# Optimization experiments

Hardware: AMD Instinct MI355X
Metric: run time of the kernel (lower is better)

The kernel has to match this reference:

```python
import jax, jax.numpy as jnp
import numpy as np
import math

N, C, W = 4, 768, 2048
H = 12            # num_attention_heads
D = C // H        # attention_head_size = 64
G = 4             # q/k/v groups


def grouped_conv1x1(x, w, b):
    # x: [N, C, W]; w: [G, C/G, C/G] (cout_per_g, cin_per_g); b: [C]
    xg = x.reshape(N, G, C // G, W)
    out = jnp.einsum('goc,ngcw->ngow', w, xg)       # [N, G, C/G, W]
    return out.reshape(N, C, W) + b[None, :, None]


def setup_inputs() -> dict:
    key = jax.random.key(0)
    ks = jax.random.split(key, 7)
    s = 1.0 / math.sqrt(C // G)
    return {
        'hidden_states': jax.random.normal(ks[0], (N, C, W), jnp.float32),
        'attention_mask': jnp.zeros((N, 1, 1, W), jnp.float32),
        'wq': jax.random.normal(ks[1], (G, C // G, C // G), jnp.float32) * s,
        'bq': jax.random.normal(ks[2], (C,), jnp.float32) * 0.02,
        'wk': jax.random.normal(ks[3], (G, C // G, C // G), jnp.float32) * s,
        'bk': jax.random.normal(ks[4], (C,), jnp.float32) * 0.02,
        'wv': jax.random.normal(ks[5], (G, C // G, C // G), jnp.float32) * s,
        'bv': jax.random.normal(ks[6], (C,), jnp.float32) * 0.02,
    }


def reference(hidden_states, attention_mask, wq, bq, wk, bk, wv, bv):
    q = grouped_conv1x1(hidden_states, wq, bq)       # [N, C, W]
    k = grouped_conv1x1(hidden_states, wk, bk)
    v = grouped_conv1x1(hidden_states, wv, bv)
    # transpose_for_scores_conv1d: [N,C,W] -> [N,H,W,D]
    q = q.reshape(N, H, D, W).transpose(0, 1, 3, 2)
    # transpose_key_for_scores_conv1d: [N,C,W] -> [N,H,D,W]
    k = k.reshape(N, H, D, W)
    v = v.reshape(N, H, D, W).transpose(0, 1, 3, 2)
    scores = jnp.einsum('nhqd,nhdk->nhqk', q, k) / math.sqrt(D)
    scores = scores + attention_mask                 # broadcast [N,1,1,W]
    probs = jax.nn.softmax(scores, axis=-1)          # dropout p=0 (eval)
    ctx = jnp.einsum('nhqk,nhkd->nhqd', probs, v)    # [N,H,W,D]
    # transpose_output_conv1d: [N,H,W,D] -> [N,C,W]
    return ctx.transpose(0, 1, 3, 2).reshape(N, C, W)
```

## Files before the change

### kernel.cpp

```cpp
#include <hip/hip_runtime.h>
#include <math.h>

typedef __attribute__((ext_vector_type(4))) float floatx4;
typedef __attribute__((ext_vector_type(8))) short shortx8;
typedef __attribute__((ext_vector_type(4))) short shortx4;

#define NB 4
#define CC 768
#define WW 2048
#define HH 12
#define DD 64
#define GG 4
#define CG 192
#define HPG 3
#define L2E 1.4426950408889634f
#define C18 0.18033688011112043f
#define MSH 11.541560327111707f
#define WSZ (GG * CG * CG)

__device__ __forceinline__ float fast_exp2(float x) {
    return __builtin_amdgcn_exp2f(x);
}

__device__ __forceinline__ short f2bf(float f) {
    union { float f; unsigned u; } v; v.f = f;
    unsigned r = v.u + 0x7fffu + ((v.u >> 16) & 1u);
    return (short)(r >> 16);
}

template<int CTRL>
__device__ __forceinline__ float dppror(float v) {
    return __int_as_float(__builtin_amdgcn_update_dpp(
        0, __float_as_int(v), CTRL, 0xf, 0xf, false));
}
__device__ __forceinline__ float rsum16(float v) {
    v += dppror<0x128>(v);
    v += dppror<0x124>(v);
    v += dppror<0x122>(v);
    v += dppror<0x121>(v);
    return v;
}

__device__ __forceinline__ void gl_lds16(const void* g, void* l) {
    __builtin_amdgcn_global_load_lds(
        (const __attribute__((address_space(1))) unsigned int*)g,
        (__attribute__((address_space(3))) unsigned int*)l, 16, 0, 0);
}

__global__ __launch_bounds__(256) void prep(
    const float* __restrict__ x,
    const float* __restrict__ wq, const float* __restrict__ wk,
    const float* __restrict__ wv,
    short* __restrict__ XTh, short* __restrict__ Wf)
{
    __shared__ short Th[64 * 72];
    const int tid = threadIdx.x;
    const int b   = blockIdx.x;

    if (b < 1536) {
        const int w0 = (b & 31) * 64;
        const int c0 = ((b >> 5) % 12) * 64;
        const int n  = b / 384;
        const int w  = tid & 63;
        const int cb = (tid >> 6) * 16;

        float xv[16];
        #pragma unroll
        for (int j = 0; j < 16; ++j)
            xv[j] = x[((size_t)n * CC + c0 + cb + j) * WW + w0 + w];

        shortx8 hi0, hi1;
        #pragma unroll
        for (int j = 0; j < 8; ++j) { hi0[j] = f2bf(xv[j]); hi1[j] = f2bf(xv[j + 8]); }
        *(shortx8*)&Th[w * 72 + cb]     = hi0;
        *(shortx8*)&Th[w * 72 + cb + 8] = hi1;
        __syncthreads();

        const int wr = tid >> 2;
        const int cc = (tid & 3) * 16;
        const size_t ro = ((size_t)n * WW + w0 + wr) * CC + c0 + cc;
        *(shortx8*)&XTh[ro]     = *(const shortx8*)&Th[wr * 72 + cc];
        *(shortx8*)&XTh[ro + 8] = *(const shortx8*)&Th[wr * 72 + cc + 8];
    } else {
        const int t = (b - 1536) * 256 + tid;
        const int g  = t / (CG * CG);
        const int r  = t - g * (CG * CG);
        const int o  = r / CG;
        const int k  = r - o * CG;
        const int off = (((g * 12 + (o >> 4)) * 6 + (k >> 5)) * 512)
                      + ((k >> 3) & 3) * 128 + (o & 15) * 8 + (k & 7);
        const float* src[3] = {wq, wk, wv};
        #pragma unroll
        for (int m = 0; m < 3; ++m)
            Wf[m * WSZ + off] = f2bf(src[m][t]);
    }
}

__global__ __launch_bounds__(256) void qkv_gemm(
    const short* __restrict__ XTh, const short* __restrict__ Wf,
    const float* __restrict__ bq, const float* __restrict__ bk,
    const float* __restrict__ bv,
    short* __restrict__ Qb, short* __restrict__ Kb, short* __restrict__ Vb)
{
    __shared__ __align__(16) char smem[26112];
    short* Xh_l = (short*)smem;

    const int lin  = blockIdx.x;
    const int xcd  = lin & 7;
    const int iw   = lin >> 3;
    const int mat  = iw % 3;
    const int tile = (iw / 3) * 8 + xcd;
    const int p0   = (tile & 31) * 64;
    const int g    = (tile >> 5) & 3;
    const int n    = tile >> 7;

    const int tid  = threadIdx.x;
    const int wid  = __builtin_amdgcn_readfirstlane(tid >> 6);
    const int lane = tid & 63;
    const int l15  = lane & 15;
    const int quad = lane >> 4;
    const int ob   = wid * 48;

    {
        const short* xhb = XTh + ((size_t)n * WW + p0) * CC + g * CG;
        #pragma unroll
        for (int rd = 0; rd < 6; ++rd) {
            const int Lb = rd * 256 + wid * 64;
            const int L  = Lb + lane;
            const int p  = (L * 2731) >> 16;
            const int sc = L - p * 24;
            const int ss = (sc & ~7) | ((sc & 7) ^ (p & 7));
            gl_lds16(xhb + (size_t)p * CC + ss * 8, &Xh_l[Lb * 8]);
        }
    }
    __syncthreads();

    floatx4 acc[3][4];
    #pragma unroll
    for (int mi = 0; mi < 3; ++mi)
        #pragma unroll
        for (int ni = 0; ni < 4; ++ni) acc[mi][ni] = (floatx4)0.0f;

    const short* wfm = Wf + (size_t)mat * WSZ + lane * 8;

    #pragma unroll
    for (int ks = 0; ks < 6; ++ks) {
        shortx8 ah[3], bh[4];
        #pragma unroll
        for (int mi = 0; mi < 3; ++mi)
            ah[mi] = *(const shortx8*)(wfm + (((g * 12 + wid * 3 + mi) * 6 + ks) << 9));
        #pragma unroll
        for (int ni = 0; ni < 4; ++ni) {
            const int p  = ni * 16 + l15;
            const int vp = (ks >> 1) * 8 + ((((ks & 1) * 4) + quad) ^ (p & 7));
            bh[ni] = *(const shortx8*)&Xh_l[(p * 24 + vp) * 8];
        }
        #pragma unroll
        for (int mi = 0; mi < 3; ++mi)
            #pragma unroll
            for (int ni = 0; ni < 4; ++ni)
                acc[mi][ni] = __builtin_amdgcn_mfma_f32_16x16x32_bf16(ah[mi], bh[ni], acc[mi][ni], 0, 0, 0);
    }

    const float* bias = (mat == 0) ? bq : (mat == 1) ? bk : bv;
    short* Y = (mat == 0) ? Qb : (mat == 1) ? Kb : Vb;

    __syncthreads();

    if (mat < 2) {
        short* T = (short*)smem;
        #pragma unroll
        for (int mi = 0; mi < 3; ++mi) {
            float4 b4 = *(const float4*)&bias[g * CG + ob + mi * 16 + quad * 4];
            const int o = ob + mi * 16 + quad * 4;
            #pragma unroll
            for (int ni = 0; ni < 4; ++ni) {
                const int p = ni * 16 + l15;
                T[p * 200 + o]     = f2bf(acc[mi][ni][0] + b4.x);
                T[p * 200 + o + 1] = f2bf(acc[mi][ni][1] + b4.y);
                T[p * 200 + o + 2] = f2bf(acc[mi][ni][2] + b4.z);
                T[p * 200 + o + 3] = f2bf(acc[mi][ni][3] + b4.w);
            }
        }
        __syncthreads();
        #pragma unroll
        for (int hc = 0; hc < HPG; ++hc) {
            const size_t nh = (size_t)n * HH + g * HPG + hc;
            #pragma unroll
            for (int half = 0; half < 2; ++half) {
                const int idx = tid + half * 256;
                const int p  = idx >> 3;
                const int dc = (idx & 7) * 8;
                *(shortx8*)&Y[(nh * WW + p0 + p) * DD + dc] =
                    *(const shortx8*)&T[p * 200 + hc * 64 + dc];
            }
        }
    } else {
        short* T = (short*)smem;
        #pragma unroll
        for (int mi = 0; mi < 3; ++mi) {
            float4 b4 = *(const float4*)&bias[g * CG + ob + mi * 16 + quad * 4];
            const int o = ob + mi * 16 + quad * 4;
            #pragma unroll
            for (int ni = 0; ni < 4; ++ni) {
                const int p = ni * 16 + l15;
                T[(o)     * 68 + p] = f2bf(acc[mi][ni][0] + b4.x);
                T[(o + 1) * 68 + p] = f2bf(acc[mi][ni][1] + b4.y);
                T[(o + 2) * 68 + p] = f2bf(acc[mi][ni][2] + b4.z);
                T[(o + 3) * 68 + p] = f2bf(acc[mi][ni][3] + b4.w);
            }
        }
        __syncthreads();
        #pragma unroll
        for (int pass = 0; pass < 6; ++pass) {
            const int idx = tid + pass * 256;
            const int o  = idx >> 3;
            const int pc = (idx & 7) * 8;
            const size_t nh = (size_t)n * HH + g * HPG + (o >> 6);
            const int d = o & 63;
            *(shortx8*)&Y[(nh * DD + d) * WW + p0 + pc] =
                *(const shortx8*)&T[o * 68 + pc];
        }
    }
}

#define PST 72
#define RST 65

__global__ __launch_bounds__(256) void attn_split(
    const short* __restrict__ Qb, const short* __restrict__ Kb,
    const short* __restrict__ Vb, const float* __restrict__ mask,
    float* __restrict__ out)
{
    __shared__ __align__(16) char smem[50176];
    short* Pl = (short*)(smem + 32768);
    float* Ml = (float*)(smem + 41984);

    const int lin  = blockIdx.x;
    const int xcd  = lin & 7;
    const int slot = lin >> 3;
    const int pair = xcd * 6 + (slot >> 5);
    const int qt   = slot & 31;
    const int n    = pair / HH;
    const int h    = pair % HH;
    const int q0   = qt * 64;

    const int tid  = threadIdx.x;
    const int wid  = __builtin_amdgcn_readfirstlane(tid >> 6);
    const int lane = tid & 63;
    const int l15  = lane & 15;
    const int quad = lane >> 4;

    const size_t nh = (size_t)n * HH + h;
    const short* Kbase = Kb + nh * WW * DD;
    const short* Vbase = Vb + nh * DD * WW;

    {
        const float* mbase = mask + (size_t)n * WW;
        #pragma unroll
        for (int i = 0; i < WW / 256; ++i)
            Ml[tid + i * 256] = fmaf(mbase[tid + i * 256], L2E, -MSH);
    }

    shortx8 qf[2];
    {
        const short* qp = Qb + (nh * WW + q0 + wid * 16 + l15) * DD + quad * 8;
        qf[0] = *(const shortx8*)(qp);
        qf[1] = *(const shortx8*)(qp + 32);
    }

    floatx4 oacc[4];
    #pragma unroll
    for (int nn2 = 0; nn2 < 4; ++nn2) oacc[nn2] = (floatx4)0.0f;
    float lst[4] = {0.f, 0.f, 0.f, 0.f};

    short* Pw = Pl + wid * 16 * PST;

    const int r0  = wid * 16 + (lane >> 3);
    const int r1  = r0 + 8;
    const int cg0 = (lane & 7) ^ (r0 & 7);
    const int cg1 = (lane & 7) ^ (r1 & 7);
    const short* kp0 = Kbase + (size_t)r0 * DD + cg0 * 8;
    const short* kp1 = Kbase + (size_t)r1 * DD + cg1 * 8;
    const short* vp0 = Vbase + (size_t)r0 * WW + cg0 * 8;
    const short* vp1 = Vbase + (size_t)r1 * WW + cg1 * 8;
    const int KR0 = (wid * 16) * 64, KR1 = (wid * 16 + 8) * 64;

    #define STAGE(j, bb)                                                      \
        do {                                                                  \
            short* ksd = (short*)(smem + (bb) * 8192);                        \
            short* vsd = (short*)(smem + 16384 + (bb) * 8192);                \
            gl_lds16(kp0 + (size_t)(j) * 64 * DD, ksd + KR0);                 \
            gl_lds16(kp1 + (size_t)(j) * 64 * DD, ksd + KR1);                 \
            gl_lds16(vp0 + (j) * 64, vsd + KR0);                              \
            gl_lds16(vp1 + (j) * 64, vsd + KR1);                              \
        } while (0)

    STAGE(0, 0);
    __syncthreads();

    for (int kt = 0; kt < WW / 64; ++kt) {
        const int bb = kt & 1;
        if (kt + 1 < WW / 64) STAGE(kt + 1, 1 - bb);

        const short* Ks_l = (const short*)(smem + bb * 8192);
        const short* Vs_l = (const short*)(smem + 16384 + bb * 8192);
        const int k0 = kt * 64;

        shortx8 kf[4][2], vf[4][2];
        #pragma unroll
        for (int jj = 0; jj < 4; ++jj) {
            const int r = 16 * jj + l15;
            #pragma unroll
            for (int hf = 0; hf < 2; ++hf)
                kf[jj][hf] = *(const shortx8*)&Ks_l[r * 64 + (((hf * 4 + quad) ^ (r & 7)) * 8)];
        }
        #pragma unroll
        for (int nn2 = 0; nn2 < 4; ++nn2) {
            const int r = 16 * nn2 + l15;
            #pragma unroll
            for (int hf = 0; hf < 2; ++hf)
                vf[nn2][hf] = *(const shortx8*)&Vs_l[r * 64 + (((hf * 4 + quad) ^ (r & 7)) * 8)];
        }
        float mv2[4];
        #pragma unroll
        for (int jj = 0; jj < 4; ++jj)
            mv2[jj] = Ml[k0 + 16 * jj + l15];

        floatx4 sacc[4];
        #pragma unroll
        for (int jj = 0; jj < 4; ++jj) {
            sacc[jj] = (floatx4)0.0f;
            sacc[jj] = __builtin_amdgcn_mfma_f32_16x16x32_bf16(qf[0], kf[jj][0], sacc[jj], 0, 0, 0);
            sacc[jj] = __builtin_amdgcn_mfma_f32_16x16x32_bf16(qf[1], kf[jj][1], sacc[jj], 0, 0, 0);
        }

        #pragma unroll
        for (int jj = 0; jj < 4; ++jj) {
            #pragma unroll
            for (int r = 0; r < 4; ++r) {
                float p = fast_exp2(fmaf(sacc[jj][r], C18, mv2[jj]));
                lst[r] += p;
                Pw[(quad * 4 + r) * PST + 16 * jj + l15] = f2bf(p);
            }
        }

        shortx8 pf0 = *(const shortx8*)&Pw[l15 * PST + quad * 8];
        shortx8 pf1 = *(const shortx8*)&Pw[l15 * PST + 32 + quad * 8];

        #pragma unroll
        for (int nn2 = 0; nn2 < 4; ++nn2) {
            oacc[nn2] = __builtin_amdgcn_mfma_f32_16x16x32_bf16(pf0, vf[nn2][0], oacc[nn2], 0, 0, 0);
            oacc[nn2] = __builtin_amdgcn_mfma_f32_16x16x32_bf16(pf1, vf[nn2][1], oacc[nn2], 0, 0, 0);
        }
        __syncthreads();
    }
    #undef STAGE

    float linv[4];
    #pragma unroll
    for (int r = 0; r < 4; ++r) linv[r] = 1.0f / rsum16(lst[r]);

    float* Ol = (float*)smem;
    #pragma unroll
    for (int nn2 = 0; nn2 < 4; ++nn2)
        #pragma unroll
        for (int r = 0; r < 4; ++r)
            Ol[(wid * 16 + quad * 4 + r) * RST + nn2 * 16 + l15] = oacc[nn2][r] * linv[r];
    __syncthreads();

    float* obase = out + (nh * DD) * WW + q0;
    #pragma unroll
    for (int it = 0; it < 4; ++it) {
        const int idx = tid + it * 256;
        const int q4 = (idx & 15) * 4;
        const int d  = idx >> 4;
        floatx4 v;
        #pragma unroll
        for (int i = 0; i < 4; ++i) v[i] = Ol[(q4 + i) * RST + d];
        *(floatx4*)&obase[(size_t)d * WW + q4] = v;
    }
}

extern "C" void kernel_launch(void* const* d_in, const int* in_sizes, int n_in,
                              void* d_out, int out_size, void* d_ws, size_t ws_size,
                              hipStream_t stream) {
    const float* x    = (const float*)d_in[0];
    const float* mask = (const float*)d_in[1];
    const float* wq   = (const float*)d_in[2];
    const float* bq   = (const float*)d_in[3];
    const float* wk   = (const float*)d_in[4];
    const float* bk   = (const float*)d_in[5];
    const float* wv   = (const float*)d_in[6];
    const float* bv   = (const float*)d_in[7];
    float* out = (float*)d_out;

    const size_t per = (size_t)NB * HH * WW * DD;
    short* Qb  = (short*)d_ws;
    short* Kb  = Qb + per;
    short* Vb  = Kb + per;
    short* XTh = Vb + per;
    short* Wfp = XTh + per;

    hipLaunchKernelGGL(prep, dim3(1536 + WSZ / 256), dim3(256), 0, stream,
                       x, wq, wk, wv, XTh, Wfp);
    hipLaunchKernelGGL(qkv_gemm, dim3(1536), dim3(256), 0, stream,
                       XTh, Wfp, bq, bk, bv, Qb, Kb, Vb);
    hipLaunchKernelGGL(attn_split, dim3(1536), dim3(256), 0, stream,
                       Qb, Kb, Vb, mask, out);
}
```

Before: 190.7 us.

## Keep softmax probabilities in registers via transposed QK MFMA and row-permuted K

Computes S^T by swapping MFMA operands and permuting the K rows loaded from LDS, so each lane's exp outputs already form the A-operand layout of the PV MFMA. The LDS round-trip for P is removed, the bf16 conversion uses packed v_cvt_pk_bf16_f32, and row sums are taken with an extra MFMA against a vector of ones instead of DPP reductions. A new LDS swizzle (swz8) and vectorized mask loads go with the new row mapping. This trades two extra MFMAs per tile and bf16-rounded row sums for fewer LDS writes and reads and less VALU work.

```diff
diff --git a/kernel.cpp b/kernel.cpp
--- a/kernel.cpp
+++ b/kernel.cpp
@@ -28,17 +28,20 @@
     return (short)(r >> 16);
 }
 
-template<int CTRL>
-__device__ __forceinline__ float dppror(float v) {
-    return __int_as_float(__builtin_amdgcn_update_dpp(
-        0, __float_as_int(v), CTRL, 0xf, 0xf, false));
-}
-__device__ __forceinline__ float rsum16(float v) {
-    v += dppror<0x128>(v);
-    v += dppror<0x124>(v);
-    v += dppror<0x122>(v);
-    v += dppror<0x121>(v);
-    return v;
+__device__ __forceinline__ int cvtpk(float lo, float hi) {
+    int r;
+    asm("v_cvt_pk_bf16_f32 %0, %1, %2" : "=v"(r) : "v"(lo), "v"(hi));
+    return r;
+}
+
+__device__ __forceinline__ shortx8 mk8(int a, int b, int c, int d) {
+    union { int i[4]; shortx8 h; } u;
+    u.i[0] = a; u.i[1] = b; u.i[2] = c; u.i[3] = d;
+    return u.h;
+}
+
+__device__ __forceinline__ int swz8(int r) {
+    return (((r & 7) * 2) + ((r >> 3) & 1)) & 7;
 }
 
 __device__ __forceinline__ void gl_lds16(const void* g, void* l) {
@@ -224,7 +227,6 @@
     }
 }
 
-#define PST 72
 #define RST 65
 
 __global__ __launch_bounds__(256) void attn_split(
@@ -232,9 +234,8 @@
     const short* __restrict__ Vb, const float* __restrict__ mask,
     float* __restrict__ out)
 {
-    __shared__ __align__(16) char smem[50176];
-    short* Pl = (short*)(smem + 32768);
-    float* Ml = (float*)(smem + 41984);
+    __shared__ __align__(16) char smem[40960];
+    float* Ml = (float*)(smem + 32768);
 
     const int lin  = blockIdx.x;
     const int xcd  = lin & 7;
@@ -269,22 +270,26 @@
         qf[1] = *(const shortx8*)(qp + 32);
     }
 
+    shortx8 onef;
+    #pragma unroll
+    for (int j = 0; j < 8; ++j) onef[j] = (short)0x3F80;
+
     floatx4 oacc[4];
     #pragma unroll
     for (int nn2 = 0; nn2 < 4; ++nn2) oacc[nn2] = (floatx4)0.0f;
-    float lst[4] = {0.f, 0.f, 0.f, 0.f};
-
-    short* Pw = Pl + wid * 16 * PST;
+    floatx4 lsum = (floatx4)0.0f;
 
     const int r0  = wid * 16 + (lane >> 3);
     const int r1  = r0 + 8;
-    const int cg0 = (lane & 7) ^ (r0 & 7);
-    const int cg1 = (lane & 7) ^ (r1 & 7);
+    const int cg0 = (lane & 7) ^ swz8(r0);
+    const int cg1 = (lane & 7) ^ swz8(r1);
     const short* kp0 = Kbase + (size_t)r0 * DD + cg0 * 8;
     const short* kp1 = Kbase + (size_t)r1 * DD + cg1 * 8;
     const short* vp0 = Vbase + (size_t)r0 * WW + cg0 * 8;
     const short* vp1 = Vbase + (size_t)r1 * WW + cg1 * 8;
     const int KR0 = (wid * 16) * 64, KR1 = (wid * 16 + 8) * 64;
+
+    const int rowmap = (l15 >> 2) * 8 + (l15 & 3);
 
     #define STAGE(j, bb)                                                      \
         do {                                                                  \
@@ -310,56 +315,62 @@
         shortx8 kf[4][2], vf[4][2];
         #pragma unroll
         for (int jj = 0; jj < 4; ++jj) {
-            const int r = 16 * jj + l15;
+            const int rp = ((jj >> 1) * 32) + ((jj & 1) * 4) + rowmap;
             #pragma unroll
             for (int hf = 0; hf < 2; ++hf)
-                kf[jj][hf] = *(const shortx8*)&Ks_l[r * 64 + (((hf * 4 + quad) ^ (r & 7)) * 8)];
+                kf[jj][hf] = *(const shortx8*)&Ks_l[rp * 64 + (((hf * 4 + quad) ^ swz8(rp)) * 8)];
         }
         #pragma unroll
         for (int nn2 = 0; nn2 < 4; ++nn2) {
             const int r = 16 * nn2 + l15;
             #pragma unroll
             for (int hf = 0; hf < 2; ++hf)
-                vf[nn2][hf] = *(const shortx8*)&Vs_l[r * 64 + (((hf * 4 + quad) ^ (r & 7)) * 8)];
-        }
-        float mv2[4];
-        #pragma unroll
-        for (int jj = 0; jj < 4; ++jj)
-            mv2[jj] = Ml[k0 + 16 * jj + l15];
+                vf[nn2][hf] = *(const shortx8*)&Vs_l[r * 64 + (((hf * 4 + quad) ^ swz8(r)) * 8)];
+        }
+
+        floatx4 mv4[4];
+        #pragma unroll
+        for (int jj = 0; jj < 4; ++jj) {
+            const int kb = ((jj >> 1) * 32) + ((jj & 1) * 4) + quad * 8;
+            mv4[jj] = *(const floatx4*)&Ml[k0 + kb];
+        }
 
         floatx4 sacc[4];
         #pragma unroll
         for (int jj = 0; jj < 4; ++jj) {
             sacc[jj] = (floatx4)0.0f;
-            sacc[jj] = __builtin_amdgcn_mfma_f32_16x16x32_bf16(qf[0], kf[jj][0], sacc[jj], 0, 0, 0);
-            sacc[jj] = __builtin_amdgcn_mfma_f32_16x16x32_bf16(qf[1], kf[jj][1], sacc[jj], 0, 0, 0);
-        }
-
+            sacc[jj] = __builtin_amdgcn_mfma_f32_16x16x32_bf16(kf[jj][0], qf[0], sacc[jj], 0, 0, 0);
+            sacc[jj] = __builtin_amdgcn_mfma_f32_16x16x32_bf16(kf[jj][1], qf[1], sacc[jj], 0, 0, 0);
+        }
+
+        int s[4][2];
         #pragma unroll
         for (int jj = 0; jj < 4; ++jj) {
-            #pragma unroll
-            for (int r = 0; r < 4; ++r) {
-                float p = fast_exp2(fmaf(sacc[jj][r], C18, mv2[jj]));
-                lst[r] += p;
-                Pw[(quad * 4 + r) * PST + 16 * jj + l15] = f2bf(p);
-            }
-        }
-
-        shortx8 pf0 = *(const shortx8*)&Pw[l15 * PST + quad * 8];
-        shortx8 pf1 = *(const shortx8*)&Pw[l15 * PST + 32 + quad * 8];
+            float p0 = fast_exp2(fmaf(sacc[jj][0], C18, mv4[jj][0]));
+            float p1 = fast_exp2(fmaf(sacc[jj][1], C18, mv4[jj][1]));
+            float p2 = fast_exp2(fmaf(sacc[jj][2], C18, mv4[jj][2]));
+            float p3 = fast_exp2(fmaf(sacc[jj][3], C18, mv4[jj][3]));
+            s[jj][0] = cvtpk(p0, p1);
+            s[jj][1] = cvtpk(p2, p3);
+        }
+        shortx8 pf0 = mk8(s[0][0], s[0][1], s[1][0], s[1][1]);
+        shortx8 pf1 = mk8(s[2][0], s[2][1], s[3][0], s[3][1]);
 
         #pragma unroll
         for (int nn2 = 0; nn2 < 4; ++nn2) {
             oacc[nn2] = __builtin_amdgcn_mfma_f32_16x16x32_bf16(pf0, vf[nn2][0], oacc[nn2], 0, 0, 0);
             oacc[nn2] = __builtin_amdgcn_mfma_f32_16x16x32_bf16(pf1, vf[nn2][1], oacc[nn2], 0, 0, 0);
         }
+        lsum = __builtin_amdgcn_mfma_f32_16x16x32_bf16(pf0, onef, lsum, 0, 0, 0);
+        lsum = __builtin_amdgcn_mfma_f32_16x16x32_bf16(pf1, onef, lsum, 0, 0, 0);
+
         __syncthreads();
     }
     #undef STAGE
 
     float linv[4];
     #pragma unroll
-    for (int r = 0; r < 4; ++r) linv[r] = 1.0f / rsum16(lst[r]);
+    for (int r = 0; r < 4; ++r) linv[r] = 1.0f / lsum[r];
 
     float* Ol = (float*)smem;
     #pragma unroll
```

Measured after the change: 179.7 us. 1.06x faster.
